# Performance work log

Measured on AMD Instinct MI355X. Metric: run time of the kernel, lower is better.

Reference implementation:

```python
import math
import jax, jax.numpy as jnp
import numpy as np

IMAGE_SIZE = 256
RADIUS = 10.0  # radius_list=[10.0] default
EYES_POS_LIST = [[-1, -1, -1], [-1, -1, 1], [-1, 1, -1], [-1, 1, 1],
                 [1, -1, -1], [1, -1, 1], [1, 1, -1], [1, 1, 1]]


def _pre_matrix(view_id):
    # projection_matrix @ look_at(eyes, 0, up=(0,0,1)), orthographic branch
    eyes = np.array(EYES_POS_LIST[view_id], np.float32)  # eyepos_scale=1.0
    ups = np.array([0.0, 0.0, 1.0], np.float32)
    z = eyes / max(float(np.linalg.norm(eyes)), 1e-6)
    x = np.cross(ups, z)
    x = x / max(float(np.linalg.norm(x)), 1e-6)
    y = np.cross(z, x)
    orient = np.eye(4, dtype=np.float32)
    orient[0, :3] = x
    orient[1, :3] = y
    orient[2, :3] = z
    trans = np.eye(4, dtype=np.float32)
    trans[:3, 3] = -eyes
    view = orient @ trans
    z_near, z_far = 0.1, 10.0
    proj = np.diag(np.array([1.5, 1.5, -2.0 / (z_far - z_near), 1.0], np.float32))
    proj[2, 3] = (z_far + z_near) / (z_far - z_near)
    return jnp.asarray((proj @ view).astype(np.float32))


def _p2i_max(pos_ij, feat, batch_inds, background, radius):
    """Splat each point onto its (i,j) pixel footprint with a cos kernel,
    reducing with max (background as init). pos_ij in NDC [-1,1]."""
    B, C, H, W = background.shape  # C == 1
    pts = (pos_ij * 0.5 + 0.5) * jnp.array([H - 1.0, W - 1.0], pos_ij.dtype)  # [P,2] pixel coords
    r = int(math.ceil(radius))
    offs = jnp.arange(-r, r + 2)  # cover full footprint around floor(center)
    di, dj = jnp.meshgrid(offs, offs, indexing="ij")
    di = di.reshape(-1)
    dj = dj.reshape(-1)  # [K], K=(2r+2)^2
    base = jnp.floor(pts).astype(jnp.int32)  # [P,2]
    pi = base[:, :1] + di[None, :]  # [P,K]
    pj = base[:, 1:] + dj[None, :]
    d = jnp.sqrt((pi.astype(pts.dtype) - pts[:, :1]) ** 2 +
                 (pj.astype(pts.dtype) - pts[:, 1:]) ** 2)
    w = jnp.where(d <= radius, jnp.cos(d * (jnp.pi / 2.0 / radius)), 0.0)  # cos kernel
    vals = w * feat  # feat [P,1] broadcasts -> [P,K]
    valid = (pi >= 0) & (pi < H) & (pj >= 0) & (pj < W)
    flat = batch_inds[:, None] * (H * W) + pi * W + pj
    flat = jnp.where(valid, flat, B * H * W)  # dump slot for out-of-bounds
    canvas = jnp.full((B * H * W + 1,), -jnp.inf, background.dtype)
    canvas = canvas.at[flat.reshape(-1)].max(vals.reshape(-1))
    return jnp.maximum(background, canvas[:-1].reshape(B, 1, H, W))


def _forward(data, view_id):
    B, N, _ = data.shape
    M = _pre_matrix(view_id)  # [4,4]
    pcd = data.reshape(-1, 3)  # [B*N,3]
    hom = pcd @ M[:, :3].T + M[:, 3][None, :]  # [B*N,4]
    xyz = hom[:, :3] / hom[:, 3:4]
    pos_ij = jnp.stack([-xyz[:, 1], xyz[:, 0]], axis=1)  # (i,j) = (-y, x)
    z = xyz[:, 2:3]
    feat = 1.0 - (z - z.min()) / (z.max() - z.min())  # [B*N,1]
    batch_inds = jnp.repeat(jnp.arange(B, dtype=jnp.int32), N)
    background = jnp.zeros((B, 1, IMAGE_SIZE, IMAGE_SIZE), data.dtype)
    return _p2i_max(pos_ij, feat, batch_inds, background, RADIUS)


def setup_inputs() -> dict:
    key = jax.random.key(0)
    data = jax.random.normal(key, (32, 4096, 3), dtype=jnp.float32) * 0.5  # unit-ish cloud
    return {"data": data, "view_id": 0}


def reference(data, view_id):
    return _forward(data, view_id)
```

## Files before the change

kernel.cpp:

```cpp
#include <hip/hip_runtime.h>
#include <math.h>

#define IMG_H 256
#define IMG_W 256
#define NBATCH 32
#define NPER 4096
#define NPTS (NBATCH * NPER)
#define STRIP 8
#define NSTRIPS (IMG_H / STRIP)
#define THREADS 512
#define NWAVES (THREADS / 64)
#define PADL 19
#define ROWW 299
#define CANVAS_W (STRIP * ROWW)
#define KC  0.15707964f
#define KC3 0.47123890f
#define TMAX 2.4674011f
#define BINS (NBATCH * NSTRIPS)
#define CAP 2048
#define BBLK 512
#define SCH 512


struct Mats { float m[8][12]; };

static void build_mats(float out[8][12]) {
  static const double EYES[8][3] = {
    {-1,-1,-1},{-1,-1, 1},{-1, 1,-1},{-1, 1, 1},
    { 1,-1,-1},{ 1,-1, 1},{ 1, 1,-1},{ 1, 1, 1}};
  for (int v = 0; v < 8; ++v) {
    const double* e = EYES[v];
    double en = sqrt(e[0]*e[0] + e[1]*e[1] + e[2]*e[2]);
    if (en < 1e-6) en = 1e-6;
    double z[3] = {e[0]/en, e[1]/en, e[2]/en};
    double x[3] = {-z[1], z[0], 0.0};
    double xn = sqrt(x[0]*x[0] + x[1]*x[1]);
    if (xn < 1e-6) xn = 1e-6;
    x[0] /= xn; x[1] /= xn; x[2] = 0.0;
    double y[3] = {z[1]*x[2] - z[2]*x[1],
                   z[2]*x[0] - z[0]*x[2],
                   z[0]*x[1] - z[1]*x[0]};
    const double s  = 1.5;
    const double pz = -2.0 / (10.0 - 0.1);
    const double c3 = (10.0 + 0.1) / (10.0 - 0.1);
    double dxe = x[0]*e[0] + x[1]*e[1] + x[2]*e[2];
    double dye = y[0]*e[0] + y[1]*e[1] + y[2]*e[2];
    double dze = z[0]*e[0] + z[1]*e[1] + z[2]*e[2];
    out[v][0] = (float)(s*x[0]); out[v][1] = (float)(s*x[1]);
    out[v][2] = (float)(s*x[2]); out[v][3] = (float)(-s*dxe);
    out[v][4] = (float)(s*y[0]); out[v][5] = (float)(s*y[1]);
    out[v][6] = (float)(s*y[2]); out[v][7] = (float)(-s*dye);
    out[v][8] = (float)(pz*z[0]); out[v][9] = (float)(pz*z[1]);
    out[v][10] = (float)(pz*z[2]); out[v][11] = (float)(-pz*dze + c3);
  }
}

__global__ __launch_bounds__(256)
void bin_agg(const float* __restrict__ data,
             const int* __restrict__ view_id,
             Mats mats, unsigned int* __restrict__ cnt,
             float4* __restrict__ rec, float* __restrict__ red) {
  __shared__ unsigned int hist[NSTRIPS];
  __shared__ unsigned int base[NSTRIPS];
  __shared__ float smn[4], smx[4];

  const int tid = threadIdx.x;
  const int blk = blockIdx.x;
  const int b   = blk >> 4;
  const int p   = blk * 256 + tid;

  if (tid < NSTRIPS) hist[tid] = 0u;
  __syncthreads();

  const int v = (*view_id) & 7;
  const float* M = mats.m[v];
  float x = data[3*p+0], y = data[3*p+1], zz = data[3*p+2];
  float h1 = M[4]*x + M[5]*y + M[6]*zz + M[7];
  float pif = (-h1 * 0.5f + 0.5f) * (float)(IMG_H - 1);
  int base_i = (int)floorf(pif);
  int lo = max(base_i - 9, 0), hi = min(base_i + 10, IMG_H - 1);
  float h0 = M[0]*x + M[1]*y + M[2]*zz + M[3];
  float pjf = (h0 * 0.5f + 0.5f) * (float)(IMG_W - 1);
  int base_j = (int)floorf(pjf);
  float h2 = M[8]*x + M[9]*y + M[10]*zz + M[11];

  bool valid = (lo <= hi) & (base_j >= -10) & (base_j <= IMG_W + 8);
  int s0 = lo >> 3, s1 = valid ? (hi >> 3) : (lo >> 3) - 1;

  unsigned fr0 = 0xFFFFFFFFu, fr1 = 0xFFFFFFFFu,
           fr2 = 0xFFFFFFFFu, fr3 = 0xFFFFFFFFu;
  if (valid) {
    fr0 = atomicAdd(&hist[s0], 1u) | ((unsigned)s0 << 16);
    if (s0 + 1 <= s1) fr1 = atomicAdd(&hist[s0 + 1], 1u) | ((unsigned)(s0 + 1) << 16);
    if (s0 + 2 <= s1) fr2 = atomicAdd(&hist[s0 + 2], 1u) | ((unsigned)(s0 + 2) << 16);
    if (s0 + 3 <= s1) fr3 = atomicAdd(&hist[s0 + 3], 1u) | ((unsigned)(s0 + 3) << 16);
  }

  float zmn = h2, zmx = h2;
#pragma unroll
  for (int m = 32; m >= 1; m >>= 1) {
    zmn = fminf(zmn, __shfl_xor(zmn, m, 64));
    zmx = fmaxf(zmx, __shfl_xor(zmx, m, 64));
  }
  if ((tid & 63) == 0) { smn[tid >> 6] = zmn; smx[tid >> 6] = zmx; }

  __syncthreads();

  if (tid < NSTRIPS) {
    unsigned h = hist[tid];
    base[tid] = h ? atomicAdd(&cnt[b * NSTRIPS + tid], h) : 0u;
  }
  if (tid == 64) {
    red[blk] = fminf(fminf(smn[0], smn[1]), fminf(smn[2], smn[3]));
    red[BBLK + blk] = fmaxf(fmaxf(smx[0], smx[1]), fmaxf(smx[2], smx[3]));
  }
  __syncthreads();

  if (valid) {
    float fj_s = ((float)(base_j - 9) - pjf) * KC;
#pragma unroll
    for (int k = 0; k < 4; ++k) {
      unsigned fr = (k == 0) ? fr0 : (k == 1) ? fr1 : (k == 2) ? fr2 : fr3;
      if (fr != 0xFFFFFFFFu) {
        int s = (int)(fr >> 16);
        unsigned idx = base[s] + (fr & 0xFFFFu);
        if (idx < CAP) {
          int i0 = max(lo, s * STRIP);
          int i1 = min(hi, s * STRIP + (STRIP - 1));
          int rows = i1 - i0 + 1;
          int basew = (i0 - s * STRIP) * ROWW + (base_j + 10);
          unsigned meta = ((unsigned)rows << 12) | (unsigned)basew;
          float fi_s = ((float)i0 - pif) * KC;
          rec[(size_t)(b * NSTRIPS + s) * CAP + idx] =
              make_float4(fi_s, fj_s, h2, __uint_as_float(meta));
        }
      }
    }
  }
}

__global__ __launch_bounds__(THREADS, 8)
void splat_drain(const unsigned int* __restrict__ cnt,
                 const float4* __restrict__ rec,
                 const float* __restrict__ red,
                 float* __restrict__ out) {
  __shared__ unsigned int canvas[CANVAS_W];
  __shared__ float4 stage[SCH];
  __shared__ float zred[2];

  const int tid  = threadIdx.x;
  const int lane = tid & 63;
  const int wid  = tid >> 6;
  const int b    = blockIdx.y;
  const int strip = (blockIdx.x + b) & 31;
  const int bin  = b * NSTRIPS + strip;

  for (int i = tid; i < CANVAS_W; i += THREADS) canvas[i] = 0u;

  if (tid < 64) {
    float a = INFINITY, c = -INFINITY;
#pragma unroll
    for (int k = 0; k < BBLK / 64; ++k) {
      a = fminf(a, red[tid + 64 * k]);
      c = fmaxf(c, red[BBLK + tid + 64 * k]);
    }
#pragma unroll
    for (int m = 32; m >= 1; m >>= 1) {
      a = fminf(a, __shfl_xor(a, m, 64));
      c = fmaxf(c, __shfl_xor(c, m, 64));
    }
    if (tid == 0) { zred[0] = a; zred[1] = c; }
  }
  __syncthreads();

  const float zmin = zred[0];
  const float zinv = 1.0f / (zred[1] - zmin);

  const int n = min((int)cnt[bin], CAP);
  const float4* recs = rec + (size_t)bin * CAP;

  const int r_l   = (lane * 3277) >> 16;
  const int col_l = lane - r_l * 20;
  const float col_kc = (float)col_l * KC;
  const float r_kc   = (float)r_l * KC;

  for (int c0 = 0; c0 < n; c0 += SCH) {
    const int m = min(SCH, n - c0);
    if (c0) __syncthreads();
    for (int i = tid; i < m; i += THREADS) stage[i] = recs[c0 + i];
    __syncthreads();

    if (lane < 60) {
      for (int e = wid; e < m; e += NWAVES) {
        float4 Q = stage[e];
        float fi_s = Q.x, fj_s = Q.y;
        unsigned meta = __float_as_uint(Q.w);
        float feat = fmaxf(1.0f - (Q.z - zmin) * zinv, 0.0f);
        int basew = (int)(meta & 0xFFFu);
        int rows  = (int)(meta >> 12);
        float dy = col_kc + fj_s;
        float dy2 = dy * dy;
        float dx = r_kc + fi_s;
        unsigned int* ptr = canvas + (basew + r_l * ROWW + col_l);
        int rb = 0;
        for (; rb + 3 <= rows; rb += 3) {
          float t = fminf(__builtin_fmaf(dx, dx, dy2), TMAX);
          float w = __builtin_fmaf(t,
                      __builtin_fmaf(t,
                        __builtin_fmaf(t,
                          __builtin_fmaf(t, 2.4801587e-5f, -1.3888889e-3f),
                          4.1666668e-2f),
                        -0.5f),
                      1.0f);
          atomicMax(ptr, __float_as_uint(w * feat));
          dx += KC3;
          ptr += 3 * ROWW;
        }
        if (rb < rows) {
          int row = min(rb + r_l, rows - 1);
          float dxt = __builtin_fmaf((float)row, KC, fi_s);
          float t = fminf(__builtin_fmaf(dxt, dxt, dy2), TMAX);
          float w = __builtin_fmaf(t,
                      __builtin_fmaf(t,
                        __builtin_fmaf(t,
                          __builtin_fmaf(t, 2.4801587e-5f, -1.3888889e-3f),
                          4.1666668e-2f),
                        -0.5f),
                      1.0f);
          atomicMax(canvas + (basew + row * ROWW + col_l),
                    __float_as_uint(w * feat));
        }
      }
    }
  }

  __syncthreads();
  float* outb = out + ((size_t)b * IMG_H + strip * STRIP) * IMG_W;
#pragma unroll
  for (int i = tid; i < STRIP * IMG_W; i += THREADS) {
    int r = i >> 8, col = i & 255;
    outb[i] = __uint_as_float(canvas[r * ROWW + PADL + col]);
  }
}

extern "C" void kernel_launch(void* const* d_in, const int* in_sizes, int n_in,
                              void* d_out, int out_size, void* d_ws, size_t ws_size,
                              hipStream_t stream) {
  const float* data = (const float*)d_in[0];
  const int* view_id = (const int*)d_in[1];
  float* out = (float*)d_out;

  unsigned int* cnt = (unsigned int*)d_ws;
  float* red = (float*)((char*)d_ws + 4096);
  float4* rec = (float4*)((char*)d_ws + 8192);

  Mats mats;
  build_mats(mats.m);

  hipMemsetAsync(cnt, 0, BINS * sizeof(unsigned int), stream);
  bin_agg<<<BBLK, 256, 0, stream>>>(data, view_id, mats, cnt, rec, red);
  dim3 grid(NSTRIPS, NBATCH);
  splat_drain<<<grid, THREADS, 0, stream>>>(cnt, rec, red, out);
}
```

Measured before the change: 38.36 us.

## Replace global atomic bin counters with per-block windows and prefix-scan in drain

Each binning block now writes its per-strip histogram and records into a private fixed window (16 windows per batch/strip, 256 entries each) instead of reserving slots with global atomicAdd. The drain kernel prefix-scans the 16 window counts to compact records into shared staging. This removes the memset launch, the global atomics and a block barrier. In exchange the drain does scattered window gathers, and the per-bin CAP clamp is gone, so workspace use grows.

```diff
diff --git a/kernel.cpp b/kernel.cpp
--- a/kernel.cpp
+++ b/kernel.cpp
@@ -16,9 +16,9 @@
 #define KC  0.15707964f
 #define KC3 0.47123890f
 #define TMAX 2.4674011f
-#define BINS (NBATCH * NSTRIPS)
-#define CAP 2048
 #define BBLK 512
+#define WPB 16
+#define WCAP 256
 #define SCH 512
 
 
@@ -58,16 +58,16 @@
 __global__ __launch_bounds__(256)
 void bin_agg(const float* __restrict__ data,
              const int* __restrict__ view_id,
-             Mats mats, unsigned int* __restrict__ cnt,
+             Mats mats, unsigned int* __restrict__ counts,
              float4* __restrict__ rec, float* __restrict__ red) {
   __shared__ unsigned int hist[NSTRIPS];
-  __shared__ unsigned int base[NSTRIPS];
   __shared__ float smn[4], smx[4];
 
-  const int tid = threadIdx.x;
-  const int blk = blockIdx.x;
-  const int b   = blk >> 4;
-  const int p   = blk * 256 + tid;
+  const int tid  = threadIdx.x;
+  const int blk  = blockIdx.x;
+  const int b    = blk >> 4;
+  const int kblk = blk & 15;
+  const int p    = blk * 256 + tid;
 
   if (tid < NSTRIPS) hist[tid] = 0u;
   __syncthreads();
@@ -106,15 +106,11 @@
 
   __syncthreads();
 
-  if (tid < NSTRIPS) {
-    unsigned h = hist[tid];
-    base[tid] = h ? atomicAdd(&cnt[b * NSTRIPS + tid], h) : 0u;
-  }
+  if (tid < NSTRIPS) counts[blk * NSTRIPS + tid] = hist[tid];
   if (tid == 64) {
     red[blk] = fminf(fminf(smn[0], smn[1]), fminf(smn[2], smn[3]));
     red[BBLK + blk] = fmaxf(fmaxf(smx[0], smx[1]), fmaxf(smx[2], smx[3]));
   }
-  __syncthreads();
 
   if (valid) {
     float fj_s = ((float)(base_j - 9) - pjf) * KC;
@@ -123,29 +119,29 @@
       unsigned fr = (k == 0) ? fr0 : (k == 1) ? fr1 : (k == 2) ? fr2 : fr3;
       if (fr != 0xFFFFFFFFu) {
         int s = (int)(fr >> 16);
-        unsigned idx = base[s] + (fr & 0xFFFFu);
-        if (idx < CAP) {
-          int i0 = max(lo, s * STRIP);
-          int i1 = min(hi, s * STRIP + (STRIP - 1));
-          int rows = i1 - i0 + 1;
-          int basew = (i0 - s * STRIP) * ROWW + (base_j + 10);
-          unsigned meta = ((unsigned)rows << 12) | (unsigned)basew;
-          float fi_s = ((float)i0 - pif) * KC;
-          rec[(size_t)(b * NSTRIPS + s) * CAP + idx] =
-              make_float4(fi_s, fj_s, h2, __uint_as_float(meta));
-        }
+        unsigned idx = fr & 0xFFFFu;
+        int i0 = max(lo, s * STRIP);
+        int i1 = min(hi, s * STRIP + (STRIP - 1));
+        int rows = i1 - i0 + 1;
+        int basew = (i0 - s * STRIP) * ROWW + (base_j + 10);
+        unsigned meta = ((unsigned)rows << 12) | (unsigned)basew;
+        float fi_s = ((float)i0 - pif) * KC;
+        rec[((size_t)(b * NSTRIPS + s) * WPB + kblk) * WCAP + idx] =
+            make_float4(fi_s, fj_s, h2, __uint_as_float(meta));
       }
     }
   }
 }
 
 __global__ __launch_bounds__(THREADS, 8)
-void splat_drain(const unsigned int* __restrict__ cnt,
+void splat_drain(const unsigned int* __restrict__ counts,
                  const float4* __restrict__ rec,
                  const float* __restrict__ red,
                  float* __restrict__ out) {
   __shared__ unsigned int canvas[CANVAS_W];
   __shared__ float4 stage[SCH];
+  __shared__ int off[WPB + 1];
+  __shared__ int c16[WPB];
   __shared__ float zred[2];
 
   const int tid  = threadIdx.x;
@@ -170,26 +166,47 @@
       c = fmaxf(c, __shfl_xor(c, m, 64));
     }
     if (tid == 0) { zred[0] = a; zred[1] = c; }
+  } else if (tid >= 64 && tid < 80) {
+    int k = tid - 64;
+    int c = (int)counts[(b * WPB + k) * NSTRIPS + strip];
+    int s = c;
+#pragma unroll
+    for (int d = 1; d < 16; d <<= 1) {
+      int y2 = __shfl_up(s, d, 64);
+      if (k >= d) s += y2;
+    }
+    off[k] = s - c;
+    c16[k] = c;
+    if (k == 15) off[16] = s;
   }
   __syncthreads();
 
   const float zmin = zred[0];
   const float zinv = 1.0f / (zred[1] - zmin);
-
-  const int n = min((int)cnt[bin], CAP);
-  const float4* recs = rec + (size_t)bin * CAP;
+  const int n = off[16];
 
   const int r_l   = (lane * 3277) >> 16;
   const int col_l = lane - r_l * 20;
   const float col_kc = (float)col_l * KC;
   const float r_kc   = (float)r_l * KC;
 
+  const int g16 = tid >> 5;
+  const int l32 = tid & 31;
+  const float4* win = rec + ((size_t)bin * WPB + g16) * WCAP;
+  const int wlo = off[g16];
+  const int whi = wlo + c16[g16];
+
   for (int c0 = 0; c0 < n; c0 += SCH) {
-    const int m = min(SCH, n - c0);
+    const int cend = min(c0 + SCH, n);
     if (c0) __syncthreads();
-    for (int i = tid; i < m; i += THREADS) stage[i] = recs[c0 + i];
+    {
+      int lo = max(wlo, c0), hi2 = min(whi, cend);
+      for (int g = lo + l32; g < hi2; g += 32)
+        stage[g - c0] = win[g - wlo];
+    }
     __syncthreads();
 
+    const int m = cend - c0;
     if (lane < 60) {
       for (int e = wid; e < m; e += NWAVES) {
         float4 Q = stage[e];
@@ -250,15 +267,14 @@
   const int* view_id = (const int*)d_in[1];
   float* out = (float*)d_out;
 
-  unsigned int* cnt = (unsigned int*)d_ws;
-  float* red = (float*)((char*)d_ws + 4096);
-  float4* rec = (float4*)((char*)d_ws + 8192);
+  unsigned int* counts = (unsigned int*)d_ws;
+  float* red = (float*)((char*)d_ws + 65536);
+  float4* rec = (float4*)((char*)d_ws + 131072);
 
   Mats mats;
   build_mats(mats.m);
 
-  hipMemsetAsync(cnt, 0, BINS * sizeof(unsigned int), stream);
-  bin_agg<<<BBLK, 256, 0, stream>>>(data, view_id, mats, cnt, rec, red);
+  bin_agg<<<BBLK, 256, 0, stream>>>(data, view_id, mats, counts, rec, red);
   dim3 grid(NSTRIPS, NBATCH);
-  splat_drain<<<grid, THREADS, 0, stream>>>(cnt, rec, red, out);
-}
+  splat_drain<<<grid, THREADS, 0, stream>>>(counts, rec, red, out);
+}
```

Result: faster. 33.72 us (-12.1%).
